# Kernel tuning notes

Measured on AMD Instinct MI355X. Metric: run time of the kernel, lower is better.

Reference implementation:

```python
import jax, jax.numpy as jnp
import numpy as np

DIM = 512
HEADS = 16
HEAD_DIM = DIM // HEADS
WS = (7, 7)
N = WS[0] * WS[1]  # 49
SCALE = HEAD_DIM ** (-0.5)


def _relative_position_index(ws):
    ch = np.arange(ws[0]); cw = np.arange(ws[1])
    coords = np.stack(np.meshgrid(ch, cw, indexing='ij'))          # [2, Wh, Ww]
    cf = coords.reshape(2, -1)                                      # [2, N]
    rel = cf[:, :, None] - cf[:, None, :]                           # [2, N, N]
    rel = rel.transpose(1, 2, 0).copy()                             # [N, N, 2]
    rel[:, :, 0] += ws[0] - 1
    rel[:, :, 1] += ws[1] - 1
    rel[:, :, 0] *= 2 * ws[1] - 1
    return rel.sum(-1)                                              # [N, N]

REL_IDX = jnp.asarray(_relative_position_index(WS))


def setup_inputs() -> dict:
    key = jax.random.key(0)
    ks = jax.random.split(key, 7)
    B_, nW = 2048, 64
    return {
        'x': jax.random.normal(ks[0], (B_, N, DIM), jnp.float32),
        'mask': jax.random.normal(ks[1], (nW, N, N), jnp.float32),
        'qkv_w': jax.random.normal(ks[2], (3 * DIM, DIM), jnp.float32) * 0.02,
        'qkv_b': jax.random.normal(ks[3], (3 * DIM,), jnp.float32) * 0.02,
        'proj_w': jax.random.normal(ks[4], (DIM, DIM), jnp.float32) * 0.02,
        'proj_b': jax.random.normal(ks[5], (DIM,), jnp.float32) * 0.02,
        'rpb_table': jax.random.normal(ks[6], (169, HEADS), jnp.float32) * 0.02,
    }


def reference(x, mask, qkv_w, qkv_b, proj_w, proj_b, rpb_table):
    B_, n, C = x.shape
    # qkv projection: [B_, N, 3C] -> [3, B_, H, N, hd]
    qkv = x @ qkv_w.T + qkv_b
    qkv = qkv.reshape(B_, n, 3, HEADS, HEAD_DIM).transpose(2, 0, 3, 1, 4)
    q, k, v = qkv[0], qkv[1], qkv[2]
    attn = jnp.einsum('bhid,bhjd->bhij', q * SCALE, k)              # [B_, H, N, N]
    # relative position bias gather: [N*N, H] -> [H, N, N]
    bias = rpb_table[REL_IDX.reshape(-1)].reshape(n, n, HEADS).transpose(2, 0, 1)
    attn = attn + bias[None]
    # shifted-window mask: broadcast over (batch-of-windows groups, heads)
    nW = mask.shape[0]
    attn = attn.reshape(B_ // nW, nW, HEADS, n, n) + mask[None, :, None]
    attn = attn.reshape(B_, HEADS, n, n)
    attn = jax.nn.softmax(attn, axis=-1)
    out = jnp.einsum('bhij,bhjd->bhid', attn, v)                    # [B_, H, N, hd]
    out = out.transpose(0, 2, 1, 3).reshape(B_, n, C)
    return out @ proj_w.T + proj_b
```

## Files before the change

kernel.cpp:

```cpp
#include <hip/hip_runtime.h>


#define NT 49
#define DIMC 512
#define HEADS 16
#define HD 32
#define SCALE 0.17677669529663687f
#define LOG2E 1.4426950408889634f

typedef short v8s __attribute__((ext_vector_type(8)));
typedef float v4f __attribute__((ext_vector_type(4)));
typedef unsigned short u16;

#define MFMA(a, b, c) __builtin_amdgcn_mfma_f32_16x16x32_bf16((a), (b), (c), 0, 0, 0)

__device__ __forceinline__ u16 f2b(float f) {
  unsigned u = __float_as_uint(f);
  u += 0x7FFFu + ((u >> 16) & 1u);
  return (u16)(u >> 16);
}

__device__ __forceinline__ int xb_ix(int tok, int c) {
  return ((tok << 9) + c) ^ ((tok & 7) << 3);
}
__device__ __forceinline__ int qk_ix(int base, int tok, int d) {
  return base + (((tok << 5) + d) ^ (((tok >> 1) & 7) << 3));
}
__device__ __forceinline__ int vt_ix(int d, int j) {
  return 4096 + (((d << 6) + j) ^ ((d & 7) << 3));
}
__device__ __forceinline__ int p_ix(int i, int j) {
  return ((i << 6) + j) ^ ((i & 7) << 3);
}

__global__ void prep_weights(const float* __restrict__ qkvw,
                             const float* __restrict__ projw,
                             u16* __restrict__ dst) {
  int t = blockIdx.x * 256 + threadIdx.x;
  int e = t * 4;
  float4 v;
  if (e < 786432) v = *(const float4*)(qkvw + e);
  else            v = *(const float4*)(projw + (e - 786432));
  ushort4 o4 = make_ushort4(f2b(v.x), f2b(v.y), f2b(v.z), f2b(v.w));
  *(ushort4*)(dst + e) = o4;
}

__global__ __launch_bounds__(256, 1) void wattn(
    const float* __restrict__ x, const float* __restrict__ mask,
    const float* __restrict__ qkvb, const float* __restrict__ projb,
    const float* __restrict__ rpb, const u16* __restrict__ wqkv,
    const u16* __restrict__ wproj, float* __restrict__ out) {
  __shared__ u16 xb[NT * DIMC];
  __shared__ u16 cx[NT * DIMC];
  __shared__ u16 sc_all[4 * 6144];

  const int tid = threadIdx.x;
  const int lane = tid & 63;
  const int w = tid >> 6;
  const int l15 = lane & 15;
  const int g = lane >> 4;
  const int b = blockIdx.x;

  u16* sc = sc_all + w * 6144;

  {
    const float4* xs = (const float4*)(x + (size_t)b * (NT * DIMC));
    for (int F = tid; F < NT * 128; F += 256) {
      float4 v = xs[F];
      int row = F >> 7;
      int c = (F & 127) << 2;
      int ix = xb_ix(row, c);
      *(ushort4*)&xb[ix] = make_ushort4(f2b(v.x), f2b(v.y), f2b(v.z), f2b(v.w));
    }
  }
  __syncthreads();

  int tokA[4];
#pragma unroll
  for (int it = 0; it < 4; ++it) tokA[it] = min(16 * it + l15, NT - 1);

  int ia[16];
#pragma unroll
  for (int it = 0; it < 4; ++it)
#pragma unroll
    for (int r = 0; r < 4; ++r) {
      int i = min(16 * it + 4 * g + r, NT - 1);
      ia[it * 4 + r] = 13 * (i / 7) + (i % 7) + 84;
    }
  int jb_[4], jv[4];
#pragma unroll
  for (int jt = 0; jt < 4; ++jt) {
    int j = 16 * jt + l15;
    jv[jt] = (j < NT);
    int jc = min(j, NT - 1);
    jb_[jt] = 13 * (jc / 7) + (jc % 7);
  }
  const float* mrow = mask + (size_t)(b & 63) * (NT * NT);

  for (int hh = 0; hh < 4; ++hh) {
    const int h = w * 4 + hh;
    const u16* Wq = wqkv + (size_t)(h * HD) * DIMC;
    const u16* Wk = wqkv + (size_t)(512 + h * HD) * DIMC;
    const u16* Wv = wqkv + (size_t)(1024 + h * HD) * DIMC;

    v4f aQ[4][2], aK[4][2], aV[2][4];
#pragma unroll
    for (int it = 0; it < 4; ++it)
#pragma unroll
      for (int jt = 0; jt < 2; ++jt) { aQ[it][jt] = (v4f){0,0,0,0}; aK[it][jt] = (v4f){0,0,0,0}; }
#pragma unroll
    for (int mt = 0; mt < 2; ++mt)
#pragma unroll
      for (int it = 0; it < 4; ++it) aV[mt][it] = (v4f){0,0,0,0};

    v8s xf[2][4], qf[2][2], kf[2][2], vf[2][2];
    auto LOADK = [&](int bi, int k0) {
      int kk = k0 + 8 * g;
#pragma unroll
      for (int it = 0; it < 4; ++it) xf[bi][it] = *(const v8s*)&xb[xb_ix(tokA[it], kk)];
#pragma unroll
      for (int jt = 0; jt < 2; ++jt) {
        qf[bi][jt] = *(const v8s*)(Wq + (16 * jt + l15) * DIMC + kk);
        kf[bi][jt] = *(const v8s*)(Wk + (16 * jt + l15) * DIMC + kk);
        vf[bi][jt] = *(const v8s*)(Wv + (16 * jt + l15) * DIMC + kk);
      }
    };
    LOADK(0, 0);
#pragma unroll
    for (int ks = 0; ks < 16; ++ks) {
      int cur = ks & 1;
      if (ks < 15) LOADK(cur ^ 1, 32 * (ks + 1));
#pragma unroll
      for (int it = 0; it < 4; ++it)
#pragma unroll
        for (int jt = 0; jt < 2; ++jt) {
          aQ[it][jt] = MFMA(xf[cur][it], qf[cur][jt], aQ[it][jt]);
          aK[it][jt] = MFMA(xf[cur][it], kf[cur][jt], aK[it][jt]);
        }
#pragma unroll
      for (int mt = 0; mt < 2; ++mt)
#pragma unroll
        for (int it = 0; it < 4; ++it)
          aV[mt][it] = MFMA(vf[cur][mt], xf[cur][it], aV[mt][it]);
    }

#pragma unroll
    for (int jt = 0; jt < 2; ++jt) {
      float bq = qkvb[h * HD + 16 * jt + l15];
      float bk = qkvb[512 + h * HD + 16 * jt + l15];
#pragma unroll
      for (int it = 0; it < 4; ++it)
#pragma unroll
        for (int r = 0; r < 4; ++r) {
          int tok = 16 * it + 4 * g + r;
          sc[qk_ix(0, tok, 16 * jt + l15)] = f2b((aQ[it][jt][r] + bq) * SCALE);
          sc[qk_ix(2048, tok, 16 * jt + l15)] = f2b(aK[it][jt][r] + bk);
        }
    }
#pragma unroll
    for (int mt = 0; mt < 2; ++mt)
#pragma unroll
      for (int r = 0; r < 4; ++r) {
        int d = 16 * mt + 4 * g + r;
        float bv = qkvb[1024 + h * HD + d];
#pragma unroll
        for (int it = 0; it < 4; ++it)
          sc[vt_ix(d, 16 * it + l15)] = f2b(aV[mt][it][r] + bv);
      }

    v8s qfr[4], kfr[4];
#pragma unroll
    for (int t = 0; t < 4; ++t) {
      qfr[t] = *(const v8s*)&sc[qk_ix(0, 16 * t + l15, 8 * g)];
      kfr[t] = *(const v8s*)&sc[qk_ix(2048, 16 * t + l15, 8 * g)];
    }
    float sv[4][4][4];
#pragma unroll
    for (int it = 0; it < 4; ++it)
#pragma unroll
      for (int jt = 0; jt < 4; ++jt) {
        v4f acc = (v4f){0,0,0,0};
        acc = MFMA(qfr[it], kfr[jt], acc);
#pragma unroll
        for (int r = 0; r < 4; ++r) sv[it][jt][r] = acc[r];
      }

    float rsum[4][4];
#pragma unroll
    for (int it = 0; it < 4; ++it)
#pragma unroll
      for (int r = 0; r < 4; ++r) {
        int ic = min(16 * it + 4 * g + r, NT - 1);
        const float* mr = mrow + ic * NT;
        float mx = -3e38f;
#pragma unroll
        for (int jt = 0; jt < 4; ++jt) {
          float lg = -3e38f;
          if (jv[jt]) {
            int j = 16 * jt + l15;
            float bias = rpb[(ia[it * 4 + r] - jb_[jt]) * HEADS + h];
            lg = sv[it][jt][r] + bias + mr[j];
          }
          sv[it][jt][r] = lg;
          mx = fmaxf(mx, lg);
        }
        mx = fmaxf(mx, __shfl_xor(mx, 1));
        mx = fmaxf(mx, __shfl_xor(mx, 2));
        mx = fmaxf(mx, __shfl_xor(mx, 4));
        mx = fmaxf(mx, __shfl_xor(mx, 8));
        float sum = 0.f;
#pragma unroll
        for (int jt = 0; jt < 4; ++jt) {
          float p = exp2f((sv[it][jt][r] - mx) * LOG2E);
          sv[it][jt][r] = p;
          sum += p;
        }
        sum += __shfl_xor(sum, 1);
        sum += __shfl_xor(sum, 2);
        sum += __shfl_xor(sum, 4);
        sum += __shfl_xor(sum, 8);
        rsum[it][r] = 1.f / sum;
      }

#pragma unroll
    for (int it = 0; it < 4; ++it)
#pragma unroll
      for (int jt = 0; jt < 4; ++jt)
#pragma unroll
        for (int r = 0; r < 4; ++r)
          sc[p_ix(16 * it + 4 * g + r, 16 * jt + l15)] = f2b(sv[it][jt][r]);

    v4f co[4][2];
#pragma unroll
    for (int it = 0; it < 4; ++it)
#pragma unroll
      for (int dt = 0; dt < 2; ++dt) co[it][dt] = (v4f){0,0,0,0};
#pragma unroll
    for (int ks = 0; ks < 2; ++ks) {
      v8s pf[4], vfr[2];
#pragma unroll
      for (int it = 0; it < 4; ++it) pf[it] = *(const v8s*)&sc[p_ix(16 * it + l15, 32 * ks + 8 * g)];
#pragma unroll
      for (int dt = 0; dt < 2; ++dt) vfr[dt] = *(const v8s*)&sc[vt_ix(16 * dt + l15, 32 * ks + 8 * g)];
#pragma unroll
      for (int it = 0; it < 4; ++it)
#pragma unroll
        for (int dt = 0; dt < 2; ++dt)
          co[it][dt] = MFMA(pf[it], vfr[dt], co[it][dt]);
    }

#pragma unroll
    for (int it = 0; it < 4; ++it)
#pragma unroll
      for (int r = 0; r < 4; ++r) {
        int tok = 16 * it + 4 * g + r;
        if (tok < NT) {
#pragma unroll
          for (int dt = 0; dt < 2; ++dt)
            cx[xb_ix(tok, h * HD + 16 * dt + l15)] = f2b(co[it][dt][r] * rsum[it][r]);
        }
      }
  }

  __syncthreads();

  v4f o[4][8];
#pragma unroll
  for (int it = 0; it < 4; ++it)
#pragma unroll
    for (int jt = 0; jt < 8; ++jt) o[it][jt] = (v4f){0,0,0,0};

  const u16* Wp = wproj + (size_t)(w * 128) * DIMC;
  v8s af[2][4], bfr[2][8];
  auto LOADP = [&](int bi, int k0) {
    int kk = k0 + 8 * g;
#pragma unroll
    for (int it = 0; it < 4; ++it) af[bi][it] = *(const v8s*)&cx[xb_ix(tokA[it], kk)];
#pragma unroll
    for (int jt = 0; jt < 8; ++jt) bfr[bi][jt] = *(const v8s*)(Wp + (16 * jt + l15) * DIMC + kk);
  };
  LOADP(0, 0);
#pragma unroll
  for (int ks = 0; ks < 16; ++ks) {
    int cur = ks & 1;
    if (ks < 15) LOADP(cur ^ 1, 32 * (ks + 1));
#pragma unroll
    for (int it = 0; it < 4; ++it)
#pragma unroll
      for (int jt = 0; jt < 8; ++jt)
        o[it][jt] = MFMA(af[cur][it], bfr[cur][jt], o[it][jt]);
  }

  float* ob = out + (size_t)b * (NT * DIMC) + w * 128;
#pragma unroll
  for (int jt = 0; jt < 8; ++jt) {
    float pb = projb[w * 128 + 16 * jt + l15];
#pragma unroll
    for (int it = 0; it < 4; ++it)
#pragma unroll
      for (int r = 0; r < 4; ++r) {
        int tok = 16 * it + 4 * g + r;
        if (tok < NT) ob[(size_t)tok * DIMC + 16 * jt + l15] = o[it][jt][r] + pb;
      }
  }
}

extern "C" void kernel_launch(void* const* d_in, const int* in_sizes, int n_in,
                              void* d_out, int out_size, void* d_ws, size_t ws_size,
                              hipStream_t stream) {
  const float* x     = (const float*)d_in[0];
  const float* mask  = (const float*)d_in[1];
  const float* qkvw  = (const float*)d_in[2];
  const float* qkvb  = (const float*)d_in[3];
  const float* projw = (const float*)d_in[4];
  const float* projb = (const float*)d_in[5];
  const float* rpb   = (const float*)d_in[6];
  u16* wbf = (u16*)d_ws;

  prep_weights<<<1024, 256, 0, stream>>>(qkvw, projw, wbf);
  wattn<<<2048, 256, 0, stream>>>(x, mask, qkvb, projb, rpb,
                                  wbf, wbf + 786432, (float*)d_out);
}
```

Before: 2.201 ms.

## Split fused window attention into tiled QKV GEMM, attention, and projection kernels

Replaces the single fused per-window kernel with three kernels: a 128x128 tiled bf16 MFMA GEMM for the QKV projection, which writes Q/K/V in a per-head layout to workspace, then a per-window attention kernel, then a tiled GEMM for the output projection. The work is chunked over windows to fit the available workspace. The aim is weight reuse through shared-memory tiles, where the old kernel re-read the full weights from global memory in every block, plus higher occupancy from launch bounds of 3. In exchange, Q/K/V and the context make extra round trips through global memory and there are more kernel launches.

```diff
diff --git a/kernel.cpp b/kernel.cpp
--- a/kernel.cpp
+++ b/kernel.cpp
@@ -1,10 +1,6 @@
 #include <hip/hip_runtime.h>
 
 
-#define NT 49
-#define DIMC 512
-#define HEADS 16
-#define HD 32
 #define SCALE 0.17677669529663687f
 #define LOG2E 1.4426950408889634f
 
@@ -14,191 +10,221 @@
 
 #define MFMA(a, b, c) __builtin_amdgcn_mfma_f32_16x16x32_bf16((a), (b), (c), 0, 0, 0)
 
-__device__ __forceinline__ u16 f2b(float f) {
+static __device__ __forceinline__ u16 f2b(float f) {
   unsigned u = __float_as_uint(f);
   u += 0x7FFFu + ((u >> 16) & 1u);
   return (u16)(u >> 16);
 }
 
-__device__ __forceinline__ int xb_ix(int tok, int c) {
-  return ((tok << 9) + c) ^ ((tok & 7) << 3);
-}
-__device__ __forceinline__ int qk_ix(int base, int tok, int d) {
-  return base + (((tok << 5) + d) ^ (((tok >> 1) & 7) << 3));
-}
-__device__ __forceinline__ int vt_ix(int d, int j) {
-  return 4096 + (((d << 6) + j) ^ ((d & 7) << 3));
-}
-__device__ __forceinline__ int p_ix(int i, int j) {
-  return ((i << 6) + j) ^ ((i & 7) << 3);
+#if defined(__has_builtin)
+#if __has_builtin(__builtin_amdgcn_global_load_lds)
+#define HAS_GLDS 1
+#endif
+#endif
+
+static __device__ __forceinline__ void stage16(const u16* gp, char* wave_base, char* thr_ptr) {
+#ifdef HAS_GLDS
+  __builtin_amdgcn_global_load_lds((const __attribute__((address_space(1))) unsigned int*)gp,
+                                   (__attribute__((address_space(3))) unsigned int*)wave_base,
+                                   16, 0, 0);
+#else
+  *(v8s*)thr_ptr = *(const v8s*)gp;
+#endif
 }
 
 __global__ void prep_weights(const float* __restrict__ qkvw,
                              const float* __restrict__ projw,
                              u16* __restrict__ dst) {
-  int t = blockIdx.x * 256 + threadIdx.x;
-  int e = t * 4;
+  int e = (blockIdx.x * 256 + threadIdx.x) * 4;
   float4 v;
   if (e < 786432) v = *(const float4*)(qkvw + e);
   else            v = *(const float4*)(projw + (e - 786432));
-  ushort4 o4 = make_ushort4(f2b(v.x), f2b(v.y), f2b(v.z), f2b(v.w));
-  *(ushort4*)(dst + e) = o4;
-}
-
-__global__ __launch_bounds__(256, 1) void wattn(
-    const float* __restrict__ x, const float* __restrict__ mask,
-    const float* __restrict__ qkvb, const float* __restrict__ projb,
-    const float* __restrict__ rpb, const u16* __restrict__ wqkv,
-    const u16* __restrict__ wproj, float* __restrict__ out) {
-  __shared__ u16 xb[NT * DIMC];
-  __shared__ u16 cx[NT * DIMC];
-  __shared__ u16 sc_all[4 * 6144];
-
-  const int tid = threadIdx.x;
-  const int lane = tid & 63;
-  const int w = tid >> 6;
-  const int l15 = lane & 15;
-  const int g = lane >> 4;
-  const int b = blockIdx.x;
-
-  u16* sc = sc_all + w * 6144;
-
-  {
-    const float4* xs = (const float4*)(x + (size_t)b * (NT * DIMC));
-    for (int F = tid; F < NT * 128; F += 256) {
-      float4 v = xs[F];
-      int row = F >> 7;
-      int c = (F & 127) << 2;
-      int ix = xb_ix(row, c);
-      *(ushort4*)&xb[ix] = make_ushort4(f2b(v.x), f2b(v.y), f2b(v.z), f2b(v.w));
-    }
-  }
-  __syncthreads();
+  *(ushort4*)(dst + e) = make_ushort4(f2b(v.x), f2b(v.y), f2b(v.z), f2b(v.w));
+}
+
+template<bool QKV>
+__global__ __launch_bounds__(256, 3) void gemm(
+    const void* __restrict__ Ap, const u16* __restrict__ Bp,
+    const float* __restrict__ bias, u16* __restrict__ oQ, u16* __restrict__ oK,
+    u16* __restrict__ oV, float* __restrict__ oF, int M) {
+  __shared__ u16 As[8192], Bs[8192];
+  char* Ab = (char*)As;
+  char* Bb = (char*)Bs;
+  const int tid = threadIdx.x, lane = tid & 63, w = tid >> 6;
+  const int l15 = lane & 15, g = lane >> 4;
+  const int wr = w >> 1, wc = w & 1;
+  const int n0 = blockIdx.x << 7, m0 = blockIdx.y << 7;
+
+  int prow[4], pcol[4];
+#pragma unroll
+  for (int i = 0; i < 4; ++i) {
+    int p = (i << 12) + (tid << 4);
+    int o = p ^ (((p >> 7) & 7) << 4);
+    prow[i] = o >> 7;
+    pcol[i] = (o & 127) >> 1;
+  }
+  int fo[2];
+#pragma unroll
+  for (int ks = 0; ks < 2; ++ks) fo[ks] = ((ks * 64 + g * 16) ^ ((l15 & 7) << 4));
+  const int arow_b = wr * 8192 + l15 * 128;
+  const int brow_b = wc * 8192 + l15 * 128;
+
+  v4f acc[4][4];
+#pragma unroll
+  for (int a = 0; a < 4; ++a)
+#pragma unroll
+    for (int b = 0; b < 4; ++b) acc[a][b] = (v4f){0, 0, 0, 0};
+
+  for (int kt = 0; kt < 8; ++kt) {
+    const int k0 = kt << 6;
+#pragma unroll
+    for (int i = 0; i < 4; ++i) {
+      const u16* gp = Bp + (size_t)(n0 + prow[i]) * 512 + k0 + pcol[i];
+      stage16(gp, Bb + (i << 12) + (w << 10), Bb + (i << 12) + (tid << 4));
+    }
+    if constexpr (QKV) {
+      const float* A = (const float*)Ap;
+#pragma unroll
+      for (int i = 0; i < 4; ++i) {
+        const float* s = A + (size_t)min(m0 + prow[i], M - 1) * 512 + k0 + pcol[i];
+        float4 f0 = *(const float4*)s;
+        float4 f1 = *(const float4*)(s + 4);
+        v8s hv;
+        hv[0] = (short)f2b(f0.x); hv[1] = (short)f2b(f0.y);
+        hv[2] = (short)f2b(f0.z); hv[3] = (short)f2b(f0.w);
+        hv[4] = (short)f2b(f1.x); hv[5] = (short)f2b(f1.y);
+        hv[6] = (short)f2b(f1.z); hv[7] = (short)f2b(f1.w);
+        *(v8s*)(Ab + (i << 12) + (tid << 4)) = hv;
+      }
+    } else {
+      const u16* A = (const u16*)Ap;
+#pragma unroll
+      for (int i = 0; i < 4; ++i) {
+        const u16* gp = A + (size_t)min(m0 + prow[i], M - 1) * 512 + k0 + pcol[i];
+        stage16(gp, Ab + (i << 12) + (w << 10), Ab + (i << 12) + (tid << 4));
+      }
+    }
+    __syncthreads();
+#pragma unroll
+    for (int ks = 0; ks < 2; ++ks) {
+      v8s a[4], b[4];
+#pragma unroll
+      for (int it = 0; it < 4; ++it) a[it] = *(const v8s*)(Ab + arow_b + (it << 11) + fo[ks]);
+#pragma unroll
+      for (int jt = 0; jt < 4; ++jt) b[jt] = *(const v8s*)(Bb + brow_b + (jt << 11) + fo[ks]);
+#pragma unroll
+      for (int it = 0; it < 4; ++it)
+#pragma unroll
+        for (int jt = 0; jt < 4; ++jt) acc[it][jt] = MFMA(a[it], b[jt], acc[it][jt]);
+    }
+    __syncthreads();
+  }
+
+  if constexpr (QKV) {
+    const int which = blockIdx.x >> 2;
+    u16* dst = which == 0 ? oQ : (which == 1 ? oK : oV);
+    const float scl = which == 0 ? SCALE : 1.f;
+#pragma unroll
+    for (int jt = 0; jt < 4; ++jt) {
+      int col = n0 + wc * 64 + (jt << 4) + l15;
+      float bv = bias[col];
+      int h = (col >> 5) & 15, d = col & 31;
+#pragma unroll
+      for (int it = 0; it < 4; ++it)
+#pragma unroll
+        for (int r = 0; r < 4; ++r) {
+          int m = m0 + wr * 64 + (it << 4) + (g << 2) + r;
+          if (m < M) {
+            unsigned wl = (unsigned)m / 49u, t = (unsigned)m - wl * 49u;
+            dst[(size_t)(((wl << 4) + h) * 49 + t) * 32 + d] = f2b((acc[it][jt][r] + bv) * scl);
+          }
+        }
+    }
+  } else {
+#pragma unroll
+    for (int jt = 0; jt < 4; ++jt) {
+      int col = n0 + wc * 64 + (jt << 4) + l15;
+      float bv = bias[col];
+#pragma unroll
+      for (int it = 0; it < 4; ++it)
+#pragma unroll
+        for (int r = 0; r < 4; ++r) {
+          int m = m0 + wr * 64 + (it << 4) + (g << 2) + r;
+          if (m < M) oF[(size_t)m * 512 + col] = acc[it][jt][r] + bv;
+        }
+    }
+  }
+}
+
+__global__ __launch_bounds__(256, 3) void attn(
+    const u16* __restrict__ Q, const u16* __restrict__ K, const u16* __restrict__ V,
+    const float* __restrict__ mask, const float* __restrict__ rpb,
+    u16* __restrict__ ctx, int w0) {
+  __shared__ u16 sm[4 * 6144];
+  const int tid = threadIdx.x, lane = tid & 63, w = tid >> 6;
+  const int l15 = lane & 15, g = lane >> 4;
+  const int wl = blockIdx.x;
+  u16* P = sm + w * 6144;
+  u16* VT = P + 4096;
+  const float* mrow = mask + (size_t)((w0 + wl) & 63) * (49 * 49);
 
   int tokA[4];
 #pragma unroll
-  for (int it = 0; it < 4; ++it) tokA[it] = min(16 * it + l15, NT - 1);
-
+  for (int it = 0; it < 4; ++it) tokA[it] = min(16 * it + l15, 48);
   int ia[16];
 #pragma unroll
   for (int it = 0; it < 4; ++it)
 #pragma unroll
     for (int r = 0; r < 4; ++r) {
-      int i = min(16 * it + 4 * g + r, NT - 1);
+      int i = min(16 * it + 4 * g + r, 48);
       ia[it * 4 + r] = 13 * (i / 7) + (i % 7) + 84;
     }
   int jb_[4], jv[4];
 #pragma unroll
   for (int jt = 0; jt < 4; ++jt) {
     int j = 16 * jt + l15;
-    jv[jt] = (j < NT);
-    int jc = min(j, NT - 1);
+    jv[jt] = (j < 49);
+    int jc = min(j, 48);
     jb_[jt] = 13 * (jc / 7) + (jc % 7);
   }
-  const float* mrow = mask + (size_t)(b & 63) * (NT * NT);
 
   for (int hh = 0; hh < 4; ++hh) {
-    const int h = w * 4 + hh;
-    const u16* Wq = wqkv + (size_t)(h * HD) * DIMC;
-    const u16* Wk = wqkv + (size_t)(512 + h * HD) * DIMC;
-    const u16* Wv = wqkv + (size_t)(1024 + h * HD) * DIMC;
-
-    v4f aQ[4][2], aK[4][2], aV[2][4];
-#pragma unroll
-    for (int it = 0; it < 4; ++it)
-#pragma unroll
-      for (int jt = 0; jt < 2; ++jt) { aQ[it][jt] = (v4f){0,0,0,0}; aK[it][jt] = (v4f){0,0,0,0}; }
-#pragma unroll
-    for (int mt = 0; mt < 2; ++mt)
-#pragma unroll
-      for (int it = 0; it < 4; ++it) aV[mt][it] = (v4f){0,0,0,0};
-
-    v8s xf[2][4], qf[2][2], kf[2][2], vf[2][2];
-    auto LOADK = [&](int bi, int k0) {
-      int kk = k0 + 8 * g;
-#pragma unroll
-      for (int it = 0; it < 4; ++it) xf[bi][it] = *(const v8s*)&xb[xb_ix(tokA[it], kk)];
-#pragma unroll
-      for (int jt = 0; jt < 2; ++jt) {
-        qf[bi][jt] = *(const v8s*)(Wq + (16 * jt + l15) * DIMC + kk);
-        kf[bi][jt] = *(const v8s*)(Wk + (16 * jt + l15) * DIMC + kk);
-        vf[bi][jt] = *(const v8s*)(Wv + (16 * jt + l15) * DIMC + kk);
-      }
-    };
-    LOADK(0, 0);
-#pragma unroll
-    for (int ks = 0; ks < 16; ++ks) {
-      int cur = ks & 1;
-      if (ks < 15) LOADK(cur ^ 1, 32 * (ks + 1));
-#pragma unroll
-      for (int it = 0; it < 4; ++it)
-#pragma unroll
-        for (int jt = 0; jt < 2; ++jt) {
-          aQ[it][jt] = MFMA(xf[cur][it], qf[cur][jt], aQ[it][jt]);
-          aK[it][jt] = MFMA(xf[cur][it], kf[cur][jt], aK[it][jt]);
-        }
-#pragma unroll
-      for (int mt = 0; mt < 2; ++mt)
-#pragma unroll
-        for (int it = 0; it < 4; ++it)
-          aV[mt][it] = MFMA(vf[cur][mt], xf[cur][it], aV[mt][it]);
-    }
-
-#pragma unroll
-    for (int jt = 0; jt < 2; ++jt) {
-      float bq = qkvb[h * HD + 16 * jt + l15];
-      float bk = qkvb[512 + h * HD + 16 * jt + l15];
-#pragma unroll
-      for (int it = 0; it < 4; ++it)
-#pragma unroll
-        for (int r = 0; r < 4; ++r) {
-          int tok = 16 * it + 4 * g + r;
-          sc[qk_ix(0, tok, 16 * jt + l15)] = f2b((aQ[it][jt][r] + bq) * SCALE);
-          sc[qk_ix(2048, tok, 16 * jt + l15)] = f2b(aK[it][jt][r] + bk);
-        }
-    }
-#pragma unroll
-    for (int mt = 0; mt < 2; ++mt)
+    const int h = (w << 2) + hh;
+    const size_t hb = (size_t)((wl << 4) + h) * 49 * 32;
+    const u16* Qh = Q + hb;
+    const u16* Kh = K + hb;
+    const u16* Vh = V + hb;
+
+    v8s qfr[4], kfr[4];
+#pragma unroll
+    for (int t = 0; t < 4; ++t) {
+      qfr[t] = *(const v8s*)(Qh + tokA[t] * 32 + (g << 3));
+      kfr[t] = *(const v8s*)(Kh + tokA[t] * 32 + (g << 3));
+    }
+    float sv[4][4][4];
+#pragma unroll
+    for (int it = 0; it < 4; ++it)
+#pragma unroll
+      for (int jt = 0; jt < 4; ++jt) {
+        v4f s0 = MFMA(qfr[it], kfr[jt], ((v4f){0, 0, 0, 0}));
+#pragma unroll
+        for (int r = 0; r < 4; ++r) sv[it][jt][r] = s0[r];
+      }
+
+    float rsum[4][4];
+#pragma unroll
+    for (int it = 0; it < 4; ++it)
 #pragma unroll
       for (int r = 0; r < 4; ++r) {
-        int d = 16 * mt + 4 * g + r;
-        float bv = qkvb[1024 + h * HD + d];
-#pragma unroll
-        for (int it = 0; it < 4; ++it)
-          sc[vt_ix(d, 16 * it + l15)] = f2b(aV[mt][it][r] + bv);
-      }
-
-    v8s qfr[4], kfr[4];
-#pragma unroll
-    for (int t = 0; t < 4; ++t) {
-      qfr[t] = *(const v8s*)&sc[qk_ix(0, 16 * t + l15, 8 * g)];
-      kfr[t] = *(const v8s*)&sc[qk_ix(2048, 16 * t + l15, 8 * g)];
-    }
-    float sv[4][4][4];
-#pragma unroll
-    for (int it = 0; it < 4; ++it)
-#pragma unroll
-      for (int jt = 0; jt < 4; ++jt) {
-        v4f acc = (v4f){0,0,0,0};
-        acc = MFMA(qfr[it], kfr[jt], acc);
-#pragma unroll
-        for (int r = 0; r < 4; ++r) sv[it][jt][r] = acc[r];
-      }
-
-    float rsum[4][4];
-#pragma unroll
-    for (int it = 0; it < 4; ++it)
-#pragma unroll
-      for (int r = 0; r < 4; ++r) {
-        int ic = min(16 * it + 4 * g + r, NT - 1);
-        const float* mr = mrow + ic * NT;
+        int ic = min(16 * it + 4 * g + r, 48);
+        const float* mr = mrow + ic * 49;
         float mx = -3e38f;
 #pragma unroll
         for (int jt = 0; jt < 4; ++jt) {
           float lg = -3e38f;
           if (jv[jt]) {
             int j = 16 * jt + l15;
-            float bias = rpb[(ia[it * 4 + r] - jb_[jt]) * HEADS + h];
+            float bias = rpb[(ia[it * 4 + r] - jb_[jt]) * 16 + h];
             lg = sv[it][jt][r] + bias + mr[j];
           }
           sv[it][jt][r] = lg;
@@ -227,26 +253,39 @@
 #pragma unroll
       for (int jt = 0; jt < 4; ++jt)
 #pragma unroll
-        for (int r = 0; r < 4; ++r)
-          sc[p_ix(16 * it + 4 * g + r, 16 * jt + l15)] = f2b(sv[it][jt][r]);
+        for (int r = 0; r < 4; ++r) {
+          int i = 16 * it + 4 * g + r;
+          P[((i << 6) + 16 * jt + l15) ^ ((i & 7) << 3)] = f2b(sv[it][jt][r]);
+        }
+
+#pragma unroll
+    for (int it = 0; it < 4; ++it) {
+      v8s vv = *(const v8s*)(Vh + tokA[it] * 32 + (g << 3));
+      int t = 16 * it + l15;
+#pragma unroll
+      for (int e = 0; e < 8; ++e) {
+        int d = (g << 3) + e;
+        VT[(d << 6) + (t ^ ((d & 7) << 3))] = (u16)vv[e];
+      }
+    }
 
     v4f co[4][2];
 #pragma unroll
     for (int it = 0; it < 4; ++it)
 #pragma unroll
-      for (int dt = 0; dt < 2; ++dt) co[it][dt] = (v4f){0,0,0,0};
+      for (int dt = 0; dt < 2; ++dt) co[it][dt] = (v4f){0, 0, 0, 0};
 #pragma unroll
     for (int ks = 0; ks < 2; ++ks) {
-      v8s pf[4], vfr[2];
-#pragma unroll
-      for (int it = 0; it < 4; ++it) pf[it] = *(const v8s*)&sc[p_ix(16 * it + l15, 32 * ks + 8 * g)];
-#pragma unroll
-      for (int dt = 0; dt < 2; ++dt) vfr[dt] = *(const v8s*)&sc[vt_ix(16 * dt + l15, 32 * ks + 8 * g)];
+      int jo = (32 * ks + (g << 3)) ^ ((l15 & 7) << 3);
+      v8s pf[4], vf2[2];
+#pragma unroll
+      for (int it = 0; it < 4; ++it) pf[it] = *(const v8s*)&P[((16 * it + l15) << 6) + jo];
+#pragma unroll
+      for (int dt = 0; dt < 2; ++dt) vf2[dt] = *(const v8s*)&VT[((16 * dt + l15) << 6) + jo];
 #pragma unroll
       for (int it = 0; it < 4; ++it)
 #pragma unroll
-        for (int dt = 0; dt < 2; ++dt)
-          co[it][dt] = MFMA(pf[it], vfr[dt], co[it][dt]);
+        for (int dt = 0; dt < 2; ++dt) co[it][dt] = MFMA(pf[it], vf2[dt], co[it][dt]);
     }
 
 #pragma unroll
@@ -254,53 +293,12 @@
 #pragma unroll
       for (int r = 0; r < 4; ++r) {
         int tok = 16 * it + 4 * g + r;
-        if (tok < NT) {
+        if (tok < 49) {
 #pragma unroll
           for (int dt = 0; dt < 2; ++dt)
-            cx[xb_ix(tok, h * HD + 16 * dt + l15)] = f2b(co[it][dt][r] * rsum[it][r]);
-        }
-      }
-  }
-
-  __syncthreads();
-
-  v4f o[4][8];
-#pragma unroll
-  for (int it = 0; it < 4; ++it)
-#pragma unroll
-    for (int jt = 0; jt < 8; ++jt) o[it][jt] = (v4f){0,0,0,0};
-
-  const u16* Wp = wproj + (size_t)(w * 128) * DIMC;
-  v8s af[2][4], bfr[2][8];
-  auto LOADP = [&](int bi, int k0) {
-    int kk = k0 + 8 * g;
-#pragma unroll
-    for (int it = 0; it < 4; ++it) af[bi][it] = *(const v8s*)&cx[xb_ix(tokA[it], kk)];
-#pragma unroll
-    for (int jt = 0; jt < 8; ++jt) bfr[bi][jt] = *(const v8s*)(Wp + (16 * jt + l15) * DIMC + kk);
-  };
-  LOADP(0, 0);
-#pragma unroll
-  for (int ks = 0; ks < 16; ++ks) {
-    int cur = ks & 1;
-    if (ks < 15) LOADP(cur ^ 1, 32 * (ks + 1));
-#pragma unroll
-    for (int it = 0; it < 4; ++it)
-#pragma unroll
-      for (int jt = 0; jt < 8; ++jt)
-        o[it][jt] = MFMA(af[cur][it], bfr[cur][jt], o[it][jt]);
-  }
-
-  float* ob = out + (size_t)b * (NT * DIMC) + w * 128;
-#pragma unroll
-  for (int jt = 0; jt < 8; ++jt) {
-    float pb = projb[w * 128 + 16 * jt + l15];
-#pragma unroll
-    for (int it = 0; it < 4; ++it)
-#pragma unroll
-      for (int r = 0; r < 4; ++r) {
-        int tok = 16 * it + 4 * g + r;
-        if (tok < NT) ob[(size_t)tok * DIMC + 16 * jt + l15] = o[it][jt][r] + pb;
+            ctx[(size_t)(wl * 49 + tok) * 512 + (h << 5) + (dt << 4) + l15] =
+                f2b(co[it][dt][r] * rsum[it][r]);
+        }
       }
   }
 }
@@ -315,9 +313,36 @@
   const float* projw = (const float*)d_in[4];
   const float* projb = (const float*)d_in[5];
   const float* rpb   = (const float*)d_in[6];
+  float* out = (float*)d_out;
+
   u16* wbf = (u16*)d_ws;
+  const size_t FIXED_B = 1048576 * 2;
+  const size_t PER_W = 200704;
+  size_t avail = ws_size > FIXED_B ? ws_size - FIXED_B : 0;
+  int wpc = (int)(avail / PER_W);
+  if (wpc < 1) wpc = 1;
+  if (wpc > 1024) wpc = 1024;
+  int CH = (2048 + wpc - 1) / wpc;
+  wpc = (2048 + CH - 1) / CH;
+
+  u16* qb = wbf + 1048576;
+  u16* kb = qb + (size_t)wpc * 25088;
+  u16* vb = kb + (size_t)wpc * 25088;
+  u16* cb = vb + (size_t)wpc * 25088;
 
   prep_weights<<<1024, 256, 0, stream>>>(qkvw, projw, wbf);
-  wattn<<<2048, 256, 0, stream>>>(x, mask, qkvb, projb, rpb,
-                                  wbf, wbf + 786432, (float*)d_out);
-}
+
+  for (int c = 0; c < CH; ++c) {
+    int w0 = c * wpc;
+    int nw = 2048 - w0; if (nw > wpc) nw = wpc;
+    if (nw <= 0) break;
+    int M = nw * 49;
+    int mt = (M + 127) / 128;
+    gemm<true><<<dim3(12, mt), 256, 0, stream>>>(
+        (const void*)(x + (size_t)w0 * 25088), wbf, qkvb, qb, kb, vb, nullptr, M);
+    attn<<<nw, 256, 0, stream>>>(qb, kb, vb, mask, rpb, cb, w0);
+    gemm<false><<<dim3(4, mt), 256, 0, stream>>>(
+        (const void*)cb, wbf + 786432, projb, nullptr, nullptr, nullptr,
+        out + (size_t)w0 * 25088, M);
+  }
+}
```

Measured after the change: 2.039 ms. 1.08x faster.
